# Kernel tuning notes

Hardware: AMD Instinct MI355X
Metric: run time of the kernel (lower is better)

## Reference

```python
import jax, jax.numpy as jnp
import numpy as np

N_NODES = 10000
T = 8
F_IN = 4
H1 = 16
HEADS = 4
H2 = 32
G = 32
PW = 16
E = 160000


def _gat(x, src, dst, W, a_src, a_dst, b, concat):
    # x: [T, N, Fin]; PyG GATConv (eval mode, dropout inactive), self-loops already in src/dst
    t, n, _ = x.shape
    heads, c = a_src.shape
    z = (x @ W).reshape(t, n, heads, c)                      # [T,N,H,C]
    asrc = jnp.einsum('tnhc,hc->tnh', z, a_src)
    adst = jnp.einsum('tnhc,hc->tnh', z, a_dst)
    e = jax.nn.leaky_relu(asrc[:, src] + adst[:, dst], 0.2)   # [T,E,H]
    e = e.transpose(1, 0, 2)                                  # [E,T,H]
    m = jax.ops.segment_max(e, dst, num_segments=n)           # [N,T,H]
    ex = jnp.exp(e - m[dst])
    s = jax.ops.segment_sum(ex, dst, num_segments=n)
    att = ex / s[dst]                                         # [E,T,H] softmax over in-edges of dst
    msg = z.transpose(1, 0, 2, 3)[src] * att[..., None]       # [E,T,H,C]
    out = jax.ops.segment_sum(msg, dst, num_segments=n)       # [N,T,H,C]
    out = out.transpose(1, 0, 2, 3)                           # [T,N,H,C]
    out = out.reshape(t, n, heads * c) if concat else out.mean(axis=2)
    return out + b


def _forward(dynamic, cI, cR, N, I, R, edge_index, h0,
             W1, att_src1, att_dst1, b1, W2, att_src2, att_dst2, b2,
             W_ih, W_hh, b_ih, b_hh, Wi, bi, Wr, br, Ws, bs):
    Npop = N.squeeze()
    loops = jnp.arange(N_NODES, dtype=edge_index.dtype)
    src = jnp.concatenate([edge_index[0], loops])
    dst = jnp.concatenate([edge_index[1], loops])
    x = dynamic.transpose(1, 0, 2)                            # [T,N,F] all timesteps batched
    x = jax.nn.elu(_gat(x, src, dst, W1, att_src1, att_dst1, b1, True))
    x = jax.nn.elu(_gat(x, src, dst, W2, att_src2, att_dst2, b2, False))
    cur_h = x.mean(axis=1)                                    # [T,H2]

    def gru_step(h, xt):  # torch GRUCell: gates in (r,z,n) order
        gi = W_ih @ xt + b_ih
        gh = W_hh @ h + b_hh
        ir, iz, inn = jnp.split(gi, 3)
        hr, hz, hn = jnp.split(gh, 3)
        r = jax.nn.sigmoid(ir + hr)
        zg = jax.nn.sigmoid(iz + hz)
        ng = jnp.tanh(inn + r * hn)
        hnew = (1.0 - zg) * ng + zg * h
        return hnew, hnew

    h_final, hs = jax.lax.scan(gru_step, h0[0], cur_h)        # hs: [T,G]
    hc = jnp.concatenate([hs, cI[:, None], cR[:, None]], axis=1)  # [T,G+2]
    new_I = (hc @ Wi.T + bi)[None]                            # [1,T,PW]
    new_R = (hc @ Wr.T + br)[None]
    sir = hc @ Ws.T + bs                                      # [T,2]
    alpha = jax.nn.sigmoid(sir[:, 0])
    beta = jax.nn.sigmoid(sir[:, 1])

    def sir_step(carry, _):
        lI, lR = carry
        lS = Npop - lI - lR
        dI = alpha * lI * (lS / Npop) - beta * lI
        dR = beta * lI
        # original accumulates detached increments
        return (lI + jax.lax.stop_gradient(dI), lR + jax.lax.stop_gradient(dR)), (dI, dR)

    _, (dIs, dRs) = jax.lax.scan(sir_step, (I, R), None, length=PW)  # [PW,T]
    phy_I = dIs.T[None]                                       # [1,T,PW]
    phy_R = dRs.T[None]
    return new_I, new_R, phy_I, phy_R, h_final[None]


def setup_inputs() -> dict:
    key = jax.random.key(0)
    ks = jax.random.split(key, 20)
    rn = lambda k, s, sc=0.1: (jax.random.normal(k, s) * sc).astype(jnp.float32)
    return {
        'dynamic': jax.random.normal(ks[0], (N_NODES, T, F_IN), jnp.float32),
        'cI': jax.random.uniform(ks[1], (T,), jnp.float32),
        'cR': jax.random.uniform(ks[2], (T,), jnp.float32),
        'N': jnp.ones((1,), jnp.float32) * 1e6,
        'I': jax.random.uniform(ks[3], (T,), jnp.float32) * 1e4,
        'R': jax.random.uniform(ks[4], (T,), jnp.float32) * 1e4,
        'edge_index': jax.random.randint(ks[5], (2, E), 0, N_NODES, dtype=jnp.int32),
        'h0': rn(ks[6], (1, G)),
        'W1': rn(ks[7], (F_IN, HEADS * H1)),
        'att_src1': rn(ks[8], (HEADS, H1)),
        'att_dst1': rn(ks[9], (HEADS, H1)),
        'b1': jnp.zeros((HEADS * H1,), jnp.float32),
        'W2': rn(ks[10], (HEADS * H1, H2)),
        'att_src2': rn(ks[11], (1, H2)),
        'att_dst2': rn(ks[12], (1, H2)),
        'b2': jnp.zeros((H2,), jnp.float32),
        'W_ih': rn(ks[13], (3 * G, H2)),
        'W_hh': rn(ks[14], (3 * G, G)),
        'b_ih': jnp.zeros((3 * G,), jnp.float32),
        'b_hh': jnp.zeros((3 * G,), jnp.float32),
        'Wi': rn(ks[15], (PW, G + 2)),
        'bi': jnp.zeros((PW,), jnp.float32),
        'Wr': rn(ks[16], (PW, G + 2)),
        'br': jnp.zeros((PW,), jnp.float32),
        'Ws': rn(ks[17], (2, G + 2)),
        'bs': jnp.zeros((2,), jnp.float32),
    }


def reference(dynamic, cI, cR, N, I, R, edge_index, h0,
              W1, att_src1, att_dst1, b1, W2, att_src2, att_dst2, b2,
              W_ih, W_hh, b_ih, b_hh, Wi, bi, Wr, br, Ws, bs):
    return _forward(dynamic, cI, cR, N, I, R, edge_index, h0,
                    W1, att_src1, att_dst1, b1, W2, att_src2, att_dst2, b2,
                    W_ih, W_hh, b_ih, b_hh, Wi, bi, Wr, br, Ws, bs)
```

## Files before the change

### kernel.cpp

```cpp
#include <hip/hip_runtime.h>

#define N_NODES 10000
#define T_STEPS 8
#define F_IN 4
#define H1 16
#define HEADS 4
#define H2 32
#define G 32
#define PW 16
#define E_EDGES 160000
#define CAP 64
#define NREP 128

__device__ __forceinline__ float lrelu(float x) { return x > 0.f ? x : 0.2f * x; }
__device__ __forceinline__ float eluf(float x) { return x > 0.f ? x : (expf(x) - 1.f); }
__device__ __forceinline__ float sigmoidf(float x) { return 1.f / (1.f + expf(-x)); }
__device__ __forceinline__ float g8max(float v) {
    v = fmaxf(v, __shfl_xor(v, 8));
    v = fmaxf(v, __shfl_xor(v, 16));
    v = fmaxf(v, __shfl_xor(v, 32));
    return v;
}
__device__ __forceinline__ float g8sum(float v) {
    v += __shfl_xor(v, 8);
    v += __shfl_xor(v, 16);
    v += __shfl_xor(v, 32);
    return v;
}
__device__ __forceinline__ float bf2f(unsigned int u) {
    return __uint_as_float(u << 16);
}
__device__ __forceinline__ unsigned short f2bf(float f) {
    unsigned b = __float_as_uint(f);
    return (unsigned short)((b + 0x7FFFu + ((b >> 16) & 1u)) >> 16);
}

__global__ void __launch_bounds__(256) k_scatter_att(
        const int* __restrict__ ei, int* __restrict__ cnt, int* __restrict__ colsrc,
        const float4* __restrict__ dyn, const float* __restrict__ W1,
        const float* __restrict__ as1, const float* __restrict__ ad1,
        float4* __restrict__ asrc, float4* __restrict__ adst, int gEdge) {
    if ((int)blockIdx.x < gEdge) {
        int idx = blockIdx.x * 256 + threadIdx.x;
        if (idx >= E_EDGES) return;
        int src = ei[idx];
        int dst = ei[E_EDGES + idx];
        int pos = atomicAdd(&cnt[dst], 1);
        if (pos < CAP) colsrc[(dst << 6) + pos] = src;
    } else {
        __shared__ float VA[16], VD[16];
        int tid = threadIdx.x;
        if (tid < 32) {
            int q = tid & 15, d = q >> 2, h = q & 3;
            const float* a = (tid < 16) ? as1 : ad1;
            float acc = 0.f;
#pragma unroll
            for (int c = 0; c < 16; ++c) acc += W1[d * 64 + h * 16 + c] * a[h * 16 + c];
            if (tid < 16) VA[q] = acc;
            else VD[q] = acc;
        }
        __syncthreads();
        int idx = ((int)blockIdx.x - gEdge) * 256 + tid;
        if (idx >= T_STEPS * N_NODES) return;
        const float4 x = dyn[idx];
        float4 s4, d4;
#pragma unroll
        for (int h = 0; h < 4; ++h) {
            ((float*)&s4)[h] = x.x * VA[h] + x.y * VA[4 + h] + x.z * VA[8 + h] + x.w * VA[12 + h];
            ((float*)&d4)[h] = x.x * VD[h] + x.y * VD[4 + h] + x.z * VD[8 + h] + x.w * VD[12 + h];
        }
        asrc[idx] = s4;
        adst[idx] = d4;
    }
}

__global__ void __launch_bounds__(256) k_l1_node(
        const int* __restrict__ cnt, const int* __restrict__ colsrc,
        const float4* __restrict__ asrc, const float4* __restrict__ adst,
        const float4* __restrict__ dyn, const float* __restrict__ W1,
        const float* __restrict__ b1, const float* __restrict__ W2,
        const float* __restrict__ as2, const float* __restrict__ ad2,
        unsigned short* __restrict__ z2g, float* __restrict__ asrc2,
        float* __restrict__ adst2) {
    __shared__ float sW1[256], sB1[64], sW2[64 * 32];
    __shared__ float sAs2[32], sAd2[32];
    __shared__ float sRow[4][8 * 65];
    int tid = threadIdx.x;
    for (int i = tid; i < 64 * 32; i += 256) sW2[i] = W2[i];
    if (tid < 256) sW1[tid] = W1[tid];
    if (tid < 64) sB1[tid] = b1[tid];
    if (tid < 32) { sAs2[tid] = as2[tid]; sAd2[tid] = ad2[tid]; }
    __syncthreads();

    int lane = tid & 63, wslot = tid >> 6;
    int n = blockIdx.x * 4 + wslot;
    int t = lane & 7, es = lane >> 3;
    int beg = n << 6;
    int deg = cnt[n] + 1;
    const float4 ad = adst[(n << 3) + t];

    float m0 = -1e30f, m1 = -1e30f, m2 = -1e30f, m3 = -1e30f;
    float s0 = 0.f, s1 = 0.f, s2 = 0.f, s3 = 0.f;
    float u[16];
#pragma unroll
    for (int i = 0; i < 16; ++i) u[i] = 0.f;

    for (int cb = 0; cb < deg; cb += 24) {
        int cn = deg - cb;
        if (cn > 24) cn = 24;
        int R = (cn + 7) >> 3;
        float4 lr[3], xr[3];
#pragma unroll
        for (int r = 0; r < 3; ++r) {
            lr[r] = make_float4(-1e30f, -1e30f, -1e30f, -1e30f);
            xr[r] = make_float4(0.f, 0.f, 0.f, 0.f);
        }
#pragma unroll
        for (int r = 0; r < 3; ++r) {
            if (r < R) {
                int e = cb + r * 8 + es;
                bool act = e < deg;
                int src = (e < deg - 1) ? colsrc[beg + e] : n;
                const float4 as = asrc[(src << 3) + t];
                const float4 x4 = dyn[(src << 3) + t];
                if (act) {
                    lr[r].x = lrelu(as.x + ad.x);
                    lr[r].y = lrelu(as.y + ad.y);
                    lr[r].z = lrelu(as.z + ad.z);
                    lr[r].w = lrelu(as.w + ad.w);
                    xr[r] = x4;
                }
            }
        }
        float c0 = fmaxf(fmaxf(lr[0].x, lr[1].x), lr[2].x);
        float c1 = fmaxf(fmaxf(lr[0].y, lr[1].y), lr[2].y);
        float c2 = fmaxf(fmaxf(lr[0].z, lr[1].z), lr[2].z);
        float c3 = fmaxf(fmaxf(lr[0].w, lr[1].w), lr[2].w);
        c0 = g8max(c0); c1 = g8max(c1); c2 = g8max(c2); c3 = g8max(c3);
        float nm0 = fmaxf(m0, c0), nm1 = fmaxf(m1, c1);
        float nm2 = fmaxf(m2, c2), nm3 = fmaxf(m3, c3);
        float f0 = expf(m0 - nm0), f1 = expf(m1 - nm1);
        float f2 = expf(m2 - nm2), f3 = expf(m3 - nm3);
        m0 = nm0; m1 = nm1; m2 = nm2; m3 = nm3;
#pragma unroll
        for (int i = 0; i < 16; ++i) u[i] *= (i < 4) ? f0 : (i < 8) ? f1 : (i < 12) ? f2 : f3;
        float ws0 = 0.f, ws1 = 0.f, ws2 = 0.f, ws3 = 0.f;
#pragma unroll
        for (int r = 0; r < 3; ++r) {
            float w0 = expf(lr[r].x - m0);
            float w1 = expf(lr[r].y - m1);
            float w2 = expf(lr[r].z - m2);
            float w3 = expf(lr[r].w - m3);
            ws0 += w0; ws1 += w1; ws2 += w2; ws3 += w3;
            u[0] += w0 * xr[r].x; u[1] += w0 * xr[r].y; u[2] += w0 * xr[r].z; u[3] += w0 * xr[r].w;
            u[4] += w1 * xr[r].x; u[5] += w1 * xr[r].y; u[6] += w1 * xr[r].z; u[7] += w1 * xr[r].w;
            u[8] += w2 * xr[r].x; u[9] += w2 * xr[r].y; u[10] += w2 * xr[r].z; u[11] += w2 * xr[r].w;
            u[12] += w3 * xr[r].x; u[13] += w3 * xr[r].y; u[14] += w3 * xr[r].z; u[15] += w3 * xr[r].w;
        }
        s0 = s0 * f0 + g8sum(ws0);
        s1 = s1 * f1 + g8sum(ws1);
        s2 = s2 * f2 + g8sum(ws2);
        s3 = s3 * f3 + g8sum(ws3);
    }
#pragma unroll
    for (int i = 0; i < 16; ++i) {
        float v = u[i];
        v += __shfl_xor(v, 8);
        v += __shfl_xor(v, 16);
        v += __shfl_xor(v, 32);
        u[i] = v;
    }
    int h = es >> 1;
    float uh0 = (h == 0) ? u[0] : (h == 1) ? u[4] : (h == 2) ? u[8] : u[12];
    float uh1 = (h == 0) ? u[1] : (h == 1) ? u[5] : (h == 2) ? u[9] : u[13];
    float uh2 = (h == 0) ? u[2] : (h == 1) ? u[6] : (h == 2) ? u[10] : u[14];
    float uh3 = (h == 0) ? u[3] : (h == 1) ? u[7] : (h == 2) ? u[11] : u[15];
    float sh = (h == 0) ? s0 : (h == 1) ? s1 : (h == 2) ? s2 : s3;
    float inv = 1.f / sh;
#pragma unroll
    for (int j = 0; j < 8; ++j) {
        int c = es * 8 + j;
        float acc = uh0 * sW1[c] + uh1 * sW1[64 + c] + uh2 * sW1[128 + c] + uh3 * sW1[192 + c];
        sRow[wslot][t * 65 + c] = eluf(acc * inv + sB1[c]);
    }
    __syncthreads();
    float z0 = 0.f, z1v = 0.f, z2v = 0.f, z3v = 0.f;
#pragma unroll 8
    for (int j = 0; j < 64; ++j) {
        float r = sRow[wslot][t * 65 + j];
        const float4 w4 = *reinterpret_cast<const float4*>(&sW2[j * 32 + es * 4]);
        z0 += r * w4.x; z1v += r * w4.y; z2v += r * w4.z; z3v += r * w4.w;
    }
    int wid8 = (n << 3) + t;
    unsigned int p0 = (unsigned)f2bf(z0) | ((unsigned)f2bf(z1v) << 16);
    unsigned int p1 = (unsigned)f2bf(z2v) | ((unsigned)f2bf(z3v) << 16);
    *reinterpret_cast<uint2*>(z2g + (size_t)wid8 * 32 + es * 4) = make_uint2(p0, p1);
    float pa = z0 * sAs2[es * 4] + z1v * sAs2[es * 4 + 1] + z2v * sAs2[es * 4 + 2] + z3v * sAs2[es * 4 + 3];
    float pd = z0 * sAd2[es * 4] + z1v * sAd2[es * 4 + 1] + z2v * sAd2[es * 4 + 2] + z3v * sAd2[es * 4 + 3];
    pa = g8sum(pa);
    pd = g8sum(pd);
    if (es == 0) { asrc2[wid8] = pa; adst2[wid8] = pd; }
}

__global__ void __launch_bounds__(256) k_l2_node(
        const int* __restrict__ cnt, const int* __restrict__ colsrc,
        const float* __restrict__ asrc, const float* __restrict__ adst,
        const unsigned short* __restrict__ z2, const float* __restrict__ b2,
        float* __restrict__ part) {
    __shared__ int sSrc[4][64];
    __shared__ float sW[4][64 * 8];
    __shared__ float sF[4][8], sS[4][8];
    __shared__ float sB2[32];
    __shared__ float sPart[256];
    int tid = threadIdx.x;
    if (tid < 32) sB2[tid] = b2[tid];
    sPart[tid] = 0.f;
    __syncthreads();

    int lane = tid & 63, wslot = tid >> 6;
    int n = blockIdx.x * 4 + wslot;
    int t = lane & 7, es = lane >> 3;
    int t2 = lane >> 3, cg = lane & 7;
    int beg = n << 6;
    int deg = cnt[n] + 1;
    float ad = adst[(n << 3) + t];
    const unsigned short* zb = z2 + t2 * 32 + cg * 4;

    float m = -1e30f, s = 0.f;
    float a0 = 0.f, a1 = 0.f, a2 = 0.f, a3 = 0.f;
    for (int cb = 0; cb < deg; cb += 64) {
        int cn = deg - cb;
        if (cn > 64) cn = 64;
        int R = (cn + 7) >> 3;
        float lr[8];
#pragma unroll
        for (int r = 0; r < 8; ++r) {
            lr[r] = -1e30f;
            if (r < R) {
                int e = cb + r * 8 + es;
                bool act = e < deg;
                int src = (e < deg - 1) ? colsrc[beg + e] : n;
                if (act) lr[r] = lrelu(asrc[(src << 3) + t] + ad);
                if (t == 0) sSrc[wslot][r * 8 + es] = src;
            }
        }
        float lm = lr[0];
#pragma unroll
        for (int r = 1; r < 8; ++r) lm = fmaxf(lm, lr[r]);
        lm = g8max(lm);
        float nm = fmaxf(m, lm);
        float f = expf(m - nm);
        m = nm;
        float ws = 0.f;
#pragma unroll
        for (int r = 0; r < 8; ++r) {
            if (r < R) {
                float w = expf(lr[r] - nm);
                ws += w;
                sW[wslot][(r * 8 + es) * 8 + t] = w;
            }
        }
        s = s * f + g8sum(ws);
        if (es == 0) sF[wslot][t] = f;
        float fb = sF[wslot][t2];
        a0 *= fb; a1 *= fb; a2 *= fb; a3 *= fb;
        for (int e = 0; e < cn; ++e) {
            int src = sSrc[wslot][e];
            float w = sW[wslot][e * 8 + t2];
            uint2 pz = *reinterpret_cast<const uint2*>(zb + (size_t)src * 256);
            a0 += w * bf2f(pz.x & 0xFFFFu);
            a1 += w * bf2f(pz.x >> 16);
            a2 += w * bf2f(pz.y & 0xFFFFu);
            a3 += w * bf2f(pz.y >> 16);
        }
    }
    if (es == 0) sS[wslot][t] = s;
    float invs = 1.f / sS[wslot][t2];
    int cbase = cg * 4;
    float v0 = eluf(a0 * invs + sB2[cbase]);
    float v1 = eluf(a1 * invs + sB2[cbase + 1]);
    float v2 = eluf(a2 * invs + sB2[cbase + 2]);
    float v3 = eluf(a3 * invs + sB2[cbase + 3]);
    int pidx = t2 * 32 + cbase;
    atomicAdd(&sPart[pidx], v0);
    atomicAdd(&sPart[pidx + 1], v1);
    atomicAdd(&sPart[pidx + 2], v2);
    atomicAdd(&sPart[pidx + 3], v3);
    __syncthreads();
    atomicAdd(&part[((blockIdx.x & (NREP - 1)) << 8) + tid], sPart[tid]);
}

__global__ void k_head(const float* __restrict__ part, const float* __restrict__ h0,
                       const float* __restrict__ W_ih, const float* __restrict__ W_hh,
                       const float* __restrict__ b_ih, const float* __restrict__ b_hh,
                       const float* __restrict__ Wi, const float* __restrict__ bi,
                       const float* __restrict__ Wr, const float* __restrict__ br,
                       const float* __restrict__ Ws, const float* __restrict__ bs,
                       const float* __restrict__ cI, const float* __restrict__ cR,
                       const float* __restrict__ Nptr, const float* __restrict__ Ivec,
                       const float* __restrict__ Rvec, float* __restrict__ out) {
    __shared__ float xs[256];
    __shared__ float h[32], gi[96], gh[96], hnew[32], hs[T_STEPS * 32], sirv[16];
    const float invN = 1.0f / (float)N_NODES;
    int j = threadIdx.x;
#pragma unroll
    for (int p = 0; p < 2; ++p) {
        int e = j + p * 128;
        float sum = 0.f;
        for (int r = 0; r < NREP; ++r) sum += part[r * 256 + e];
        xs[e] = sum * invN;
    }
    if (j < 32) h[j] = h0[j];
    __syncthreads();
    for (int t = 0; t < T_STEPS; ++t) {
        if (j < 96) {
            float accI = b_ih[j], accH = b_hh[j];
            for (int k = 0; k < 32; ++k) {
                accI += W_ih[j * 32 + k] * xs[t * 32 + k];
                accH += W_hh[j * 32 + k] * h[k];
            }
            gi[j] = accI;
            gh[j] = accH;
        }
        __syncthreads();
        if (j < 32) {
            float r = sigmoidf(gi[j] + gh[j]);
            float zg = sigmoidf(gi[32 + j] + gh[32 + j]);
            float ng = tanhf(gi[64 + j] + r * gh[64 + j]);
            hnew[j] = (1.f - zg) * ng + zg * h[j];
        }
        __syncthreads();
        if (j < 32) {
            h[j] = hnew[j];
            hs[t * 32 + j] = hnew[j];
        }
        __syncthreads();
    }
    if (j < 32) out[512 + j] = h[j];
    {
        int t = j >> 4, p = j & 15;
        float accI = bi[p], accR = br[p];
        for (int k = 0; k < 34; ++k) {
            float hck = (k < 32) ? hs[t * 32 + k] : (k == 32 ? cI[t] : cR[t]);
            accI += hck * Wi[p * 34 + k];
            accR += hck * Wr[p * 34 + k];
        }
        out[j] = accI;
        out[128 + j] = accR;
    }
    if (j < 16) {
        int t = j >> 1, q = j & 1;
        float acc = bs[q];
        for (int k = 0; k < 34; ++k) {
            float hck = (k < 32) ? hs[t * 32 + k] : (k == 32 ? cI[t] : cR[t]);
            acc += hck * Ws[q * 34 + k];
        }
        sirv[j] = acc;
    }
    __syncthreads();
    if (j < 8) {
        int t = j;
        float alpha = sigmoidf(sirv[2 * t]);
        float beta = sigmoidf(sirv[2 * t + 1]);
        float Np = Nptr[0];
        float lI = Ivec[t], lR = Rvec[t];
        for (int p = 0; p < PW; ++p) {
            float lS = Np - lI - lR;
            float dI = alpha * lI * (lS / Np) - beta * lI;
            float dR = beta * lI;
            out[256 + t * 16 + p] = dI;
            out[384 + t * 16 + p] = dR;
            lI += dI;
            lR += dR;
        }
    }
}

extern "C" void kernel_launch(void* const* d_in, const int* in_sizes, int n_in,
                              void* d_out, int out_size, void* d_ws, size_t ws_size,
                              hipStream_t stream) {
    const float* dyn = (const float*)d_in[0];
    const float* cI = (const float*)d_in[1];
    const float* cR = (const float*)d_in[2];
    const float* Nptr = (const float*)d_in[3];
    const float* Ivec = (const float*)d_in[4];
    const float* Rvec = (const float*)d_in[5];
    const int* ei = (const int*)d_in[6];
    const float* h0 = (const float*)d_in[7];
    const float* W1 = (const float*)d_in[8];
    const float* as1 = (const float*)d_in[9];
    const float* ad1 = (const float*)d_in[10];
    const float* b1 = (const float*)d_in[11];
    const float* W2 = (const float*)d_in[12];
    const float* as2 = (const float*)d_in[13];
    const float* ad2 = (const float*)d_in[14];
    const float* b2 = (const float*)d_in[15];
    const float* W_ih = (const float*)d_in[16];
    const float* W_hh = (const float*)d_in[17];
    const float* b_ih = (const float*)d_in[18];
    const float* b_hh = (const float*)d_in[19];
    const float* Wi = (const float*)d_in[20];
    const float* bi = (const float*)d_in[21];
    const float* Wr = (const float*)d_in[22];
    const float* br = (const float*)d_in[23];
    const float* Ws = (const float*)d_in[24];
    const float* bs = (const float*)d_in[25];
    float* out = (float*)d_out;

    char* ws = (char*)d_ws;
    size_t off = 0;
    auto alloc = [&](size_t bytes) {
        void* p = ws + off;
        off += (bytes + 255) & ~(size_t)255;
        return p;
    };
    const size_t TN = (size_t)T_STEPS * N_NODES;
    int* cnt = (int*)alloc(N_NODES * 4);
    float* part = (float*)alloc((size_t)NREP * 256 * 4);
    size_t zero_bytes = off;
    float4* asrc1 = (float4*)alloc(TN * 16);
    float4* adst1 = (float4*)alloc(TN * 16);
    unsigned short* z2 = (unsigned short*)alloc(TN * 32 * 2);
    float* asrc2 = (float*)alloc(TN * 4);
    float* adst2 = (float*)alloc(TN * 4);
    int* colsrc = (int*)alloc((size_t)N_NODES * CAP * 4);
    (void)ws_size; (void)in_sizes; (void)n_in; (void)out_size;

    const int BT = 256;
    hipMemsetAsync(cnt, 0, zero_bytes, stream);
    int gEdge = (E_EDGES + BT - 1) / BT;
    int gNode = (int)((TN + BT - 1) / BT);
    k_scatter_att<<<gEdge + gNode, BT, 0, stream>>>(ei, cnt, colsrc, (const float4*)dyn,
                                                    W1, as1, ad1, asrc1, adst1, gEdge);
    k_l1_node<<<N_NODES / 4, BT, 0, stream>>>(cnt, colsrc, asrc1, adst1,
                                              (const float4*)dyn, W1, b1, W2, as2, ad2,
                                              z2, asrc2, adst2);
    k_l2_node<<<N_NODES / 4, BT, 0, stream>>>(cnt, colsrc, asrc2, adst2, z2, b2, part);
    k_head<<<1, 128, 0, stream>>>(part, h0, W_ih, W_hh, b_ih, b_hh, Wi, bi, Wr, br, Ws, bs,
                                  cI, cR, Nptr, Ivec, Rvec, out);
}
```

Measured before the change: 193.6 us.

## Fuse layer-1 attention logits into node kernel, drop online-softmax max, merge head into L2

Layer-1 attention logits are now recomputed inside the node kernel from the projected attention vectors instead of being materialized in a separate pass. Both GAT layers drop the running-max stabilization and accumulate exp(logit) directly, so the rescaling and shuffle-max work goes away, at the cost of possible overflow with large logits. The GRU/head kernel is folded into the layer-2 kernel via a last-block-done atomic counter, which removes one launch and a serial tail. The layer-2 loop becomes a simple per-edge serial loop without shared staging.

```diff
diff --git a/kernel.cpp b/kernel.cpp
--- a/kernel.cpp
+++ b/kernel.cpp
@@ -15,12 +15,6 @@
 __device__ __forceinline__ float lrelu(float x) { return x > 0.f ? x : 0.2f * x; }
 __device__ __forceinline__ float eluf(float x) { return x > 0.f ? x : (expf(x) - 1.f); }
 __device__ __forceinline__ float sigmoidf(float x) { return 1.f / (1.f + expf(-x)); }
-__device__ __forceinline__ float g8max(float v) {
-    v = fmaxf(v, __shfl_xor(v, 8));
-    v = fmaxf(v, __shfl_xor(v, 16));
-    v = fmaxf(v, __shfl_xor(v, 32));
-    return v;
-}
 __device__ __forceinline__ float g8sum(float v) {
     v += __shfl_xor(v, 8);
     v += __shfl_xor(v, 16);
@@ -35,144 +29,87 @@
     return (unsigned short)((b + 0x7FFFu + ((b >> 16) & 1u)) >> 16);
 }
 
-__global__ void __launch_bounds__(256) k_scatter_att(
-        const int* __restrict__ ei, int* __restrict__ cnt, int* __restrict__ colsrc,
+__global__ void __launch_bounds__(256) k_scatter(
+        const int* __restrict__ ei, int* __restrict__ cnt, int* __restrict__ colsrc) {
+    int idx = blockIdx.x * 256 + threadIdx.x;
+    if (idx >= E_EDGES) return;
+    int src = ei[idx];
+    int dst = ei[E_EDGES + idx];
+    int pos = atomicAdd(&cnt[dst], 1);
+    if (pos < CAP) colsrc[(dst << 6) + pos] = src;
+}
+
+__global__ void __launch_bounds__(256) k_l1_node(
+        const int* __restrict__ cnt, const int* __restrict__ colsrc,
         const float4* __restrict__ dyn, const float* __restrict__ W1,
         const float* __restrict__ as1, const float* __restrict__ ad1,
-        float4* __restrict__ asrc, float4* __restrict__ adst, int gEdge) {
-    if ((int)blockIdx.x < gEdge) {
-        int idx = blockIdx.x * 256 + threadIdx.x;
-        if (idx >= E_EDGES) return;
-        int src = ei[idx];
-        int dst = ei[E_EDGES + idx];
-        int pos = atomicAdd(&cnt[dst], 1);
-        if (pos < CAP) colsrc[(dst << 6) + pos] = src;
-    } else {
-        __shared__ float VA[16], VD[16];
-        int tid = threadIdx.x;
-        if (tid < 32) {
-            int q = tid & 15, d = q >> 2, h = q & 3;
-            const float* a = (tid < 16) ? as1 : ad1;
-            float acc = 0.f;
-#pragma unroll
-            for (int c = 0; c < 16; ++c) acc += W1[d * 64 + h * 16 + c] * a[h * 16 + c];
-            if (tid < 16) VA[q] = acc;
-            else VD[q] = acc;
-        }
-        __syncthreads();
-        int idx = ((int)blockIdx.x - gEdge) * 256 + tid;
-        if (idx >= T_STEPS * N_NODES) return;
-        const float4 x = dyn[idx];
-        float4 s4, d4;
-#pragma unroll
-        for (int h = 0; h < 4; ++h) {
-            ((float*)&s4)[h] = x.x * VA[h] + x.y * VA[4 + h] + x.z * VA[8 + h] + x.w * VA[12 + h];
-            ((float*)&d4)[h] = x.x * VD[h] + x.y * VD[4 + h] + x.z * VD[8 + h] + x.w * VD[12 + h];
-        }
-        asrc[idx] = s4;
-        adst[idx] = d4;
-    }
-}
-
-__global__ void __launch_bounds__(256) k_l1_node(
-        const int* __restrict__ cnt, const int* __restrict__ colsrc,
-        const float4* __restrict__ asrc, const float4* __restrict__ adst,
-        const float4* __restrict__ dyn, const float* __restrict__ W1,
         const float* __restrict__ b1, const float* __restrict__ W2,
         const float* __restrict__ as2, const float* __restrict__ ad2,
         unsigned short* __restrict__ z2g, float* __restrict__ asrc2,
         float* __restrict__ adst2) {
+    __shared__ float sVA[16], sVD[16];
     __shared__ float sW1[256], sB1[64], sW2[64 * 32];
     __shared__ float sAs2[32], sAd2[32];
     __shared__ float sRow[4][8 * 65];
     int tid = threadIdx.x;
     for (int i = tid; i < 64 * 32; i += 256) sW2[i] = W2[i];
-    if (tid < 256) sW1[tid] = W1[tid];
+    sW1[tid] = W1[tid];
     if (tid < 64) sB1[tid] = b1[tid];
     if (tid < 32) { sAs2[tid] = as2[tid]; sAd2[tid] = ad2[tid]; }
+    if (tid < 32) {
+        int q = tid & 15, d = q >> 2, hh = q & 3;
+        const float* a = (tid < 16) ? as1 : ad1;
+        float acc = 0.f;
+#pragma unroll
+        for (int c = 0; c < 16; ++c) acc += W1[d * 64 + hh * 16 + c] * a[hh * 16 + c];
+        if (tid < 16) sVA[q] = acc;
+        else sVD[q] = acc;
+    }
     __syncthreads();
 
     int lane = tid & 63, wslot = tid >> 6;
     int n = blockIdx.x * 4 + wslot;
     int t = lane & 7, es = lane >> 3;
     int beg = n << 6;
-    int deg = cnt[n] + 1;
-    const float4 ad = adst[(n << 3) + t];
-
-    float m0 = -1e30f, m1 = -1e30f, m2 = -1e30f, m3 = -1e30f;
+    int dreal = cnt[n]; if (dreal > CAP) dreal = CAP;
+    int deg = dreal + 1;
+    const float4 xo = dyn[(n << 3) + t];
+    float ad0 = xo.x * sVD[0] + xo.y * sVD[4] + xo.z * sVD[8]  + xo.w * sVD[12];
+    float ad1v = xo.x * sVD[1] + xo.y * sVD[5] + xo.z * sVD[9]  + xo.w * sVD[13];
+    float ad2v = xo.x * sVD[2] + xo.y * sVD[6] + xo.z * sVD[10] + xo.w * sVD[14];
+    float ad3v = xo.x * sVD[3] + xo.y * sVD[7] + xo.z * sVD[11] + xo.w * sVD[15];
+
     float s0 = 0.f, s1 = 0.f, s2 = 0.f, s3 = 0.f;
     float u[16];
 #pragma unroll
     for (int i = 0; i < 16; ++i) u[i] = 0.f;
 
-    for (int cb = 0; cb < deg; cb += 24) {
-        int cn = deg - cb;
-        if (cn > 24) cn = 24;
-        int R = (cn + 7) >> 3;
-        float4 lr[3], xr[3];
-#pragma unroll
-        for (int r = 0; r < 3; ++r) {
-            lr[r] = make_float4(-1e30f, -1e30f, -1e30f, -1e30f);
-            xr[r] = make_float4(0.f, 0.f, 0.f, 0.f);
-        }
-#pragma unroll
-        for (int r = 0; r < 3; ++r) {
-            if (r < R) {
-                int e = cb + r * 8 + es;
-                bool act = e < deg;
-                int src = (e < deg - 1) ? colsrc[beg + e] : n;
-                const float4 as = asrc[(src << 3) + t];
-                const float4 x4 = dyn[(src << 3) + t];
-                if (act) {
-                    lr[r].x = lrelu(as.x + ad.x);
-                    lr[r].y = lrelu(as.y + ad.y);
-                    lr[r].z = lrelu(as.z + ad.z);
-                    lr[r].w = lrelu(as.w + ad.w);
-                    xr[r] = x4;
-                }
-            }
-        }
-        float c0 = fmaxf(fmaxf(lr[0].x, lr[1].x), lr[2].x);
-        float c1 = fmaxf(fmaxf(lr[0].y, lr[1].y), lr[2].y);
-        float c2 = fmaxf(fmaxf(lr[0].z, lr[1].z), lr[2].z);
-        float c3 = fmaxf(fmaxf(lr[0].w, lr[1].w), lr[2].w);
-        c0 = g8max(c0); c1 = g8max(c1); c2 = g8max(c2); c3 = g8max(c3);
-        float nm0 = fmaxf(m0, c0), nm1 = fmaxf(m1, c1);
-        float nm2 = fmaxf(m2, c2), nm3 = fmaxf(m3, c3);
-        float f0 = expf(m0 - nm0), f1 = expf(m1 - nm1);
-        float f2 = expf(m2 - nm2), f3 = expf(m3 - nm3);
-        m0 = nm0; m1 = nm1; m2 = nm2; m3 = nm3;
-#pragma unroll
-        for (int i = 0; i < 16; ++i) u[i] *= (i < 4) ? f0 : (i < 8) ? f1 : (i < 12) ? f2 : f3;
-        float ws0 = 0.f, ws1 = 0.f, ws2 = 0.f, ws3 = 0.f;
-#pragma unroll
-        for (int r = 0; r < 3; ++r) {
-            float w0 = expf(lr[r].x - m0);
-            float w1 = expf(lr[r].y - m1);
-            float w2 = expf(lr[r].z - m2);
-            float w3 = expf(lr[r].w - m3);
-            ws0 += w0; ws1 += w1; ws2 += w2; ws3 += w3;
-            u[0] += w0 * xr[r].x; u[1] += w0 * xr[r].y; u[2] += w0 * xr[r].z; u[3] += w0 * xr[r].w;
-            u[4] += w1 * xr[r].x; u[5] += w1 * xr[r].y; u[6] += w1 * xr[r].z; u[7] += w1 * xr[r].w;
-            u[8] += w2 * xr[r].x; u[9] += w2 * xr[r].y; u[10] += w2 * xr[r].z; u[11] += w2 * xr[r].w;
-            u[12] += w3 * xr[r].x; u[13] += w3 * xr[r].y; u[14] += w3 * xr[r].z; u[15] += w3 * xr[r].w;
-        }
-        s0 = s0 * f0 + g8sum(ws0);
-        s1 = s1 * f1 + g8sum(ws1);
-        s2 = s2 * f2 + g8sum(ws2);
-        s3 = s3 * f3 + g8sum(ws3);
-    }
-#pragma unroll
-    for (int i = 0; i < 16; ++i) {
-        float v = u[i];
-        v += __shfl_xor(v, 8);
-        v += __shfl_xor(v, 16);
-        v += __shfl_xor(v, 32);
-        u[i] = v;
-    }
+    for (int e0 = 0; e0 < deg; e0 += 8) {
+        int e = e0 + es;
+        bool act = e < deg;
+        int src = (e < deg - 1) ? colsrc[beg + e] : n;
+        const float4 x4 = dyn[(src << 3) + t];
+        float l0 = x4.x * sVA[0] + x4.y * sVA[4] + x4.z * sVA[8]  + x4.w * sVA[12] + ad0;
+        float l1 = x4.x * sVA[1] + x4.y * sVA[5] + x4.z * sVA[9]  + x4.w * sVA[13] + ad1v;
+        float l2 = x4.x * sVA[2] + x4.y * sVA[6] + x4.z * sVA[10] + x4.w * sVA[14] + ad2v;
+        float l3 = x4.x * sVA[3] + x4.y * sVA[7] + x4.z * sVA[11] + x4.w * sVA[15] + ad3v;
+        float w0 = act ? expf(lrelu(l0)) : 0.f;
+        float w1 = act ? expf(lrelu(l1)) : 0.f;
+        float w2 = act ? expf(lrelu(l2)) : 0.f;
+        float w3 = act ? expf(lrelu(l3)) : 0.f;
+        s0 += w0; s1 += w1; s2 += w2; s3 += w3;
+        u[0]  += w0 * x4.x; u[1]  += w0 * x4.y; u[2]  += w0 * x4.z; u[3]  += w0 * x4.w;
+        u[4]  += w1 * x4.x; u[5]  += w1 * x4.y; u[6]  += w1 * x4.z; u[7]  += w1 * x4.w;
+        u[8]  += w2 * x4.x; u[9]  += w2 * x4.y; u[10] += w2 * x4.z; u[11] += w2 * x4.w;
+        u[12] += w3 * x4.x; u[13] += w3 * x4.y; u[14] += w3 * x4.z; u[15] += w3 * x4.w;
+    }
+    s0 = g8sum(s0); s1 = g8sum(s1); s2 = g8sum(s2); s3 = g8sum(s3);
+#pragma unroll
+    for (int i = 0; i < 16; ++i) u[i] = g8sum(u[i]);
+
     int h = es >> 1;
-    float uh0 = (h == 0) ? u[0] : (h == 1) ? u[4] : (h == 2) ? u[8] : u[12];
-    float uh1 = (h == 0) ? u[1] : (h == 1) ? u[5] : (h == 2) ? u[9] : u[13];
+    float uh0 = (h == 0) ? u[0] : (h == 1) ? u[4] : (h == 2) ? u[8]  : u[12];
+    float uh1 = (h == 0) ? u[1] : (h == 1) ? u[5] : (h == 2) ? u[9]  : u[13];
     float uh2 = (h == 0) ? u[2] : (h == 1) ? u[6] : (h == 2) ? u[10] : u[14];
     float uh3 = (h == 0) ? u[3] : (h == 1) ? u[7] : (h == 2) ? u[11] : u[15];
     float sh = (h == 0) ? s0 : (h == 1) ? s1 : (h == 2) ? s2 : s3;
@@ -202,16 +139,23 @@
     if (es == 0) { asrc2[wid8] = pa; adst2[wid8] = pd; }
 }
 
-__global__ void __launch_bounds__(256) k_l2_node(
+__global__ void __launch_bounds__(256) k_l2_head(
         const int* __restrict__ cnt, const int* __restrict__ colsrc,
         const float* __restrict__ asrc, const float* __restrict__ adst,
         const unsigned short* __restrict__ z2, const float* __restrict__ b2,
-        float* __restrict__ part) {
-    __shared__ int sSrc[4][64];
-    __shared__ float sW[4][64 * 8];
-    __shared__ float sF[4][8], sS[4][8];
+        float* __restrict__ part, int* __restrict__ done,
+        const float* __restrict__ h0,
+        const float* __restrict__ W_ih, const float* __restrict__ W_hh,
+        const float* __restrict__ b_ih, const float* __restrict__ b_hh,
+        const float* __restrict__ Wi, const float* __restrict__ bi,
+        const float* __restrict__ Wr, const float* __restrict__ br,
+        const float* __restrict__ Ws, const float* __restrict__ bs,
+        const float* __restrict__ cI, const float* __restrict__ cR,
+        const float* __restrict__ Nptr, const float* __restrict__ Ivec,
+        const float* __restrict__ Rvec, float* __restrict__ out) {
     __shared__ float sB2[32];
     __shared__ float sPart[256];
+    __shared__ int sLast;
     int tid = threadIdx.x;
     if (tid < 32) sB2[tid] = b2[tid];
     sPart[tid] = 0.f;
@@ -219,63 +163,27 @@
 
     int lane = tid & 63, wslot = tid >> 6;
     int n = blockIdx.x * 4 + wslot;
-    int t = lane & 7, es = lane >> 3;
     int t2 = lane >> 3, cg = lane & 7;
     int beg = n << 6;
-    int deg = cnt[n] + 1;
-    float ad = adst[(n << 3) + t];
+    int dreal = cnt[n]; if (dreal > CAP) dreal = CAP;
+    int deg = dreal + 1;
+    float ad = adst[(n << 3) + t2];
     const unsigned short* zb = z2 + t2 * 32 + cg * 4;
 
-    float m = -1e30f, s = 0.f;
+    float s = 0.f;
     float a0 = 0.f, a1 = 0.f, a2 = 0.f, a3 = 0.f;
-    for (int cb = 0; cb < deg; cb += 64) {
-        int cn = deg - cb;
-        if (cn > 64) cn = 64;
-        int R = (cn + 7) >> 3;
-        float lr[8];
-#pragma unroll
-        for (int r = 0; r < 8; ++r) {
-            lr[r] = -1e30f;
-            if (r < R) {
-                int e = cb + r * 8 + es;
-                bool act = e < deg;
-                int src = (e < deg - 1) ? colsrc[beg + e] : n;
-                if (act) lr[r] = lrelu(asrc[(src << 3) + t] + ad);
-                if (t == 0) sSrc[wslot][r * 8 + es] = src;
-            }
-        }
-        float lm = lr[0];
-#pragma unroll
-        for (int r = 1; r < 8; ++r) lm = fmaxf(lm, lr[r]);
-        lm = g8max(lm);
-        float nm = fmaxf(m, lm);
-        float f = expf(m - nm);
-        m = nm;
-        float ws = 0.f;
-#pragma unroll
-        for (int r = 0; r < 8; ++r) {
-            if (r < R) {
-                float w = expf(lr[r] - nm);
-                ws += w;
-                sW[wslot][(r * 8 + es) * 8 + t] = w;
-            }
-        }
-        s = s * f + g8sum(ws);
-        if (es == 0) sF[wslot][t] = f;
-        float fb = sF[wslot][t2];
-        a0 *= fb; a1 *= fb; a2 *= fb; a3 *= fb;
-        for (int e = 0; e < cn; ++e) {
-            int src = sSrc[wslot][e];
-            float w = sW[wslot][e * 8 + t2];
-            uint2 pz = *reinterpret_cast<const uint2*>(zb + (size_t)src * 256);
-            a0 += w * bf2f(pz.x & 0xFFFFu);
-            a1 += w * bf2f(pz.x >> 16);
-            a2 += w * bf2f(pz.y & 0xFFFFu);
-            a3 += w * bf2f(pz.y >> 16);
-        }
-    }
-    if (es == 0) sS[wslot][t] = s;
-    float invs = 1.f / sS[wslot][t2];
+    for (int e = 0; e < deg; ++e) {
+        int src = (e < deg - 1) ? colsrc[beg + e] : n;
+        float av = asrc[(src << 3) + t2];
+        uint2 pz = *reinterpret_cast<const uint2*>(zb + (size_t)src * 256);
+        float w = expf(lrelu(av + ad));
+        s += w;
+        a0 += w * bf2f(pz.x & 0xFFFFu);
+        a1 += w * bf2f(pz.x >> 16);
+        a2 += w * bf2f(pz.y & 0xFFFFu);
+        a3 += w * bf2f(pz.y >> 16);
+    }
+    float invs = 1.f / s;
     int cbase = cg * 4;
     float v0 = eluf(a0 * invs + sB2[cbase]);
     float v1 = eluf(a1 * invs + sB2[cbase + 1]);
@@ -288,27 +196,28 @@
     atomicAdd(&sPart[pidx + 3], v3);
     __syncthreads();
     atomicAdd(&part[((blockIdx.x & (NREP - 1)) << 8) + tid], sPart[tid]);
-}
-
-__global__ void k_head(const float* __restrict__ part, const float* __restrict__ h0,
-                       const float* __restrict__ W_ih, const float* __restrict__ W_hh,
-                       const float* __restrict__ b_ih, const float* __restrict__ b_hh,
-                       const float* __restrict__ Wi, const float* __restrict__ bi,
-                       const float* __restrict__ Wr, const float* __restrict__ br,
-                       const float* __restrict__ Ws, const float* __restrict__ bs,
-                       const float* __restrict__ cI, const float* __restrict__ cR,
-                       const float* __restrict__ Nptr, const float* __restrict__ Ivec,
-                       const float* __restrict__ Rvec, float* __restrict__ out) {
+
+    __threadfence();
+    if (tid == 0) {
+        int prev = atomicAdd(done, 1);
+        sLast = (prev == (int)gridDim.x - 1) ? 1 : 0;
+    }
+    __syncthreads();
+    if (!sLast) return;
+    __threadfence();
+
     __shared__ float xs[256];
     __shared__ float h[32], gi[96], gh[96], hnew[32], hs[T_STEPS * 32], sirv[16];
     const float invN = 1.0f / (float)N_NODES;
-    int j = threadIdx.x;
-#pragma unroll
-    for (int p = 0; p < 2; ++p) {
-        int e = j + p * 128;
-        float sum = 0.f;
-        for (int r = 0; r < NREP; ++r) sum += part[r * 256 + e];
-        xs[e] = sum * invN;
+    int j = tid;
+    if (j < 128) {
+#pragma unroll
+        for (int p = 0; p < 2; ++p) {
+            int e = j + p * 128;
+            float sum = 0.f;
+            for (int r = 0; r < NREP; ++r) sum += part[r * 256 + e];
+            xs[e] = sum * invN;
+        }
     }
     if (j < 32) h[j] = h0[j];
     __syncthreads();
@@ -337,7 +246,7 @@
         __syncthreads();
     }
     if (j < 32) out[512 + j] = h[j];
-    {
+    if (j < 128) {
         int t = j >> 4, p = j & 15;
         float accI = bi[p], accR = br[p];
         for (int k = 0; k < 34; ++k) {
@@ -416,10 +325,9 @@
     };
     const size_t TN = (size_t)T_STEPS * N_NODES;
     int* cnt = (int*)alloc(N_NODES * 4);
+    int* done = (int*)alloc(4);
     float* part = (float*)alloc((size_t)NREP * 256 * 4);
     size_t zero_bytes = off;
-    float4* asrc1 = (float4*)alloc(TN * 16);
-    float4* adst1 = (float4*)alloc(TN * 16);
     unsigned short* z2 = (unsigned short*)alloc(TN * 32 * 2);
     float* asrc2 = (float*)alloc(TN * 4);
     float* adst2 = (float*)alloc(TN * 4);
@@ -429,13 +337,11 @@
     const int BT = 256;
     hipMemsetAsync(cnt, 0, zero_bytes, stream);
     int gEdge = (E_EDGES + BT - 1) / BT;
-    int gNode = (int)((TN + BT - 1) / BT);
-    k_scatter_att<<<gEdge + gNode, BT, 0, stream>>>(ei, cnt, colsrc, (const float4*)dyn,
-                                                    W1, as1, ad1, asrc1, adst1, gEdge);
-    k_l1_node<<<N_NODES / 4, BT, 0, stream>>>(cnt, colsrc, asrc1, adst1,
-                                              (const float4*)dyn, W1, b1, W2, as2, ad2,
+    k_scatter<<<gEdge, BT, 0, stream>>>(ei, cnt, colsrc);
+    k_l1_node<<<N_NODES / 4, BT, 0, stream>>>(cnt, colsrc, (const float4*)dyn,
+                                              W1, as1, ad1, b1, W2, as2, ad2,
                                               z2, asrc2, adst2);
-    k_l2_node<<<N_NODES / 4, BT, 0, stream>>>(cnt, colsrc, asrc2, adst2, z2, b2, part);
-    k_head<<<1, 128, 0, stream>>>(part, h0, W_ih, W_hh, b_ih, b_hh, Wi, bi, Wr, br, Ws, bs,
-                                  cI, cR, Nptr, Ivec, Rvec, out);
-}
+    k_l2_head<<<N_NODES / 4, BT, 0, stream>>>(cnt, colsrc, asrc2, adst2, z2, b2, part, done,
+                                              h0, W_ih, W_hh, b_ih, b_hh, Wi, bi, Wr, br,
+                                              Ws, bs, cI, cR, Nptr, Ivec, Rvec, out);
+}
```

Measured after the change: 338.1 us. 1.75x slower.
